# Performance work log

Measured on AMD Instinct MI355X. Metric: run time of the kernel, lower is better.

The kernel has to match this reference:

```python
import jax, jax.numpy as jnp
import numpy as np

EMB = 512      # embedding / LSTM input size
HID = 1024     # LSTM hidden size per direction
NTAGS = 5      # output classes
NWORDS = 50257 # vocab size
T = 4096       # sequence length (batch is hard-coded to 1 in the original)


def setup_inputs() -> dict:
    key = jax.random.key(0)
    ks = jax.random.split(key, 13)
    f32 = jnp.float32

    def gauss(k, shape, scale=0.05):
        return jax.random.normal(k, shape, f32) * scale

    return {
        "words": jax.random.randint(ks[0], (T,), 0, NWORDS),
        # torch.nn.init.uniform_(word_emb.weight, -0.25, 0.25)
        "emb": jax.random.uniform(ks[1], (NWORDS, EMB), f32, -0.25, 0.25),
        # forward-direction LSTM params (PyTorch layout, gate order i,f,g,o)
        "Wih_f": gauss(ks[2], (4 * HID, EMB)),
        "Whh_f": gauss(ks[3], (4 * HID, HID)),
        "bih_f": gauss(ks[4], (4 * HID,)),
        "bhh_f": gauss(ks[5], (4 * HID,)),
        # backward-direction LSTM params
        "Wih_b": gauss(ks[6], (4 * HID, EMB)),
        "Whh_b": gauss(ks[7], (4 * HID, HID)),
        "bih_b": gauss(ks[8], (4 * HID,)),
        "bhh_b": gauss(ks[9], (4 * HID,)),
        # projection Linear(2*HID, NTAGS)
        "Wp": gauss(ks[10], (NTAGS, 2 * HID)),
        "bp": gauss(ks[11], (NTAGS,)),
    }


def _lstm_scan(x, Wih, Whh, bias):
    """Single-direction LSTM over x: [T, E] -> hidden states [T, H]."""
    H = Whh.shape[1]
    # precompute input-to-gate contributions for all timesteps: [T, 4H]
    xg = x @ Wih.T + bias

    def step(carry, g_in):
        h, c = carry
        gates = g_in + h @ Whh.T
        i, f, g, o = jnp.split(gates, 4)
        i = jax.nn.sigmoid(i)
        f = jax.nn.sigmoid(f)
        g = jnp.tanh(g)
        o = jax.nn.sigmoid(o)
        c = f * c + i * g
        h = o * jnp.tanh(c)
        return (h, c), h

    init = (jnp.zeros((H,), x.dtype), jnp.zeros((H,), x.dtype))
    _, hs = jax.lax.scan(step, init, xg)
    return hs


def reference(words, emb, Wih_f, Whh_f, bih_f, bhh_f,
              Wih_b, Whh_b, bih_b, bhh_b, Wp, bp):
    x = emb[words]                                        # [T, E]
    hf = _lstm_scan(x, Wih_f, Whh_f, bih_f + bhh_f)       # [T, H]
    hb = _lstm_scan(x[::-1], Wih_b, Whh_b, bih_b + bhh_b)[::-1]  # [T, H]
    # PyTorch bi-LSTM output[t] = concat(h_fwd[t], h_bwd[t]); take last step
    last = jnp.concatenate([hf[-1], hb[-1]])              # [2H]
    out = last @ Wp.T + bp                                # [NTAGS]
    return out[None, :]                                   # [1, NTAGS]
```

## Files before the change

kernel.cpp:

```cpp
#include <hip/hip_runtime.h>

typedef _Float16 half8 __attribute__((ext_vector_type(8)));
typedef float floatx4 __attribute__((ext_vector_type(4)));
typedef unsigned int u32;
typedef unsigned long long u64;
typedef u64 u64x2 __attribute__((ext_vector_type(2)));

#define T_SEQ 4096
#define EMBD  512
#define HID   1024
#define G4    4096
#define NWG   64


__device__ __forceinline__ void stage16(const void* g, void* l) {
  __builtin_amdgcn_global_load_lds((const __attribute__((address_space(1))) u32*)g,
                                   (__attribute__((address_space(3))) u32*)l, 16, 0, 0);
}

__device__ __forceinline__ float frcp(float x) {
#if __has_builtin(__builtin_amdgcn_rcpf)
  return __builtin_amdgcn_rcpf(x);
#else
  return 1.f / x;
#endif
}

__device__ __forceinline__ float fsigmoid(float x) {
  return frcp(1.f + __expf(-x));
}
__device__ __forceinline__ float ftanh(float x) {
  return fmaf(2.f, frcp(1.f + __expf(-2.f * x)), -1.f);
}


__global__ __launch_bounds__(256) void prep_kernel(
    const float* __restrict__ Whh, const float* __restrict__ Wih,
    const float* __restrict__ emb, const int* __restrict__ words,
    const float* __restrict__ bih, const float* __restrict__ bhh,
    _Float16* __restrict__ whh_h, _Float16* __restrict__ wih_h,
    _Float16* __restrict__ xh, float* __restrict__ biasf, u64* __restrict__ hg) {
  const long long S1 = (long long)G4 * HID;
  const long long S2 = (long long)G4 * EMBD;
  const long long S3 = (long long)T_SEQ * EMBD;
  const long long S4 = G4;
  const long long S5 = 1024;
  const long long tot = S1 + S2 + S3 + S4 + S5;
  long long stride = (long long)gridDim.x * blockDim.x;
  for (long long i = (long long)blockIdx.x * blockDim.x + threadIdx.x; i < tot; i += stride) {
    long long j = i;
    if (j < S1) { whh_h[j] = (_Float16)Whh[j]; continue; }
    j -= S1;
    if (j < S2) { wih_h[j] = (_Float16)Wih[j]; continue; }
    j -= S2;
    if (j < S3) {
      int t = (int)(j >> 9), e = (int)(j & 511);
      xh[j] = (_Float16)emb[(long long)words[t] * EMBD + e];
      continue;
    }
    j -= S3;
    if (j < S4) { biasf[j] = bih[j] + bhh[j]; continue; }
    j -= S4;
    hg[j] = 0ull;
  }
}


__global__ __launch_bounds__(256) void xg_gemm(
    const _Float16* __restrict__ A, const _Float16* __restrict__ B,
    const float* __restrict__ biasf, float* __restrict__ C) {
  __shared__ char smem[2][2][8192];
  const int tid = threadIdx.x;
  const int lane = tid & 63;
  const int wid = tid >> 6;
  const int wy = wid >> 1, wx = wid & 1;
  const int tm = blockIdx.x * 128, tn = blockIdx.y * 128;

  floatx4 acc[4][4];
#pragma unroll
  for (int a = 0; a < 4; a++)
#pragma unroll
    for (int b = 0; b < 4; b++) acc[a][b] = (floatx4){0.f, 0.f, 0.f, 0.f};

  auto stage = [&](int buf, int kb) {
#pragma unroll
    for (int ii = 0; ii < 2; ii++) {
      int ci = tid + ii * 256;
      int r = ci >> 2, cs = ci & 3;
      int c = cs ^ (r & 3);
      const _Float16* srcA = A + (long long)(tm + r) * EMBD + kb + c * 8;
      const _Float16* srcB = B + (long long)(tn + r) * EMBD + kb + c * 8;
      char* ldsA = &smem[buf][0][(ci & ~63) << 4];
      char* ldsB = &smem[buf][1][(ci & ~63) << 4];
      stage16(srcA, ldsA);
      stage16(srcB, ldsB);
    }
  };

  stage(0, 0);
  __syncthreads();

  for (int t = 0; t < 16; t++) {
    int cur = t & 1;
    if (t < 15) stage(cur ^ 1, (t + 1) * 32);
    const char* As = smem[cur][0];
    const char* Bs = smem[cur][1];
    const int kc = lane >> 4;
    half8 af[4], bfr[4];
#pragma unroll
    for (int am = 0; am < 4; am++) {
      int r = wy * 64 + am * 16 + (lane & 15);
      af[am] = *(const half8*)(As + r * 64 + ((kc ^ (r & 3)) << 4));
    }
#pragma unroll
    for (int bn = 0; bn < 4; bn++) {
      int r = wx * 64 + bn * 16 + (lane & 15);
      bfr[bn] = *(const half8*)(Bs + r * 64 + ((kc ^ (r & 3)) << 4));
    }
#pragma unroll
    for (int am = 0; am < 4; am++)
#pragma unroll
      for (int bn = 0; bn < 4; bn++)
        acc[am][bn] = __builtin_amdgcn_mfma_f32_16x16x32_f16(af[am], bfr[bn], acc[am][bn], 0, 0, 0);
    __syncthreads();
  }

#pragma unroll
  for (int am = 0; am < 4; am++) {
    int mrow = tm + wy * 64 + am * 16 + (lane >> 4) * 4;
#pragma unroll
    for (int bn = 0; bn < 4; bn++) {
      int n = tn + wx * 64 + bn * 16 + (lane & 15);
      int r = n & 1023, g = n >> 10;
      int np = ((r >> 4) << 6) + (((r >> 2) & 3) << 4) + ((r & 3) << 2) + g;
      float bias = biasf[n];
#pragma unroll
      for (int rg = 0; rg < 4; rg++)
        C[(long long)(mrow + rg) * G4 + np] = acc[am][bn][rg] + bias;
    }
  }
}


__global__ __launch_bounds__(256, 1) void lstm_fwd(
    const _Float16* __restrict__ Whh_h, const float* __restrict__ xg,
    u64* __restrict__ hg) {
  __shared__ u32 hp[2][512];
  const int tid = threadIdx.x;
  const int lane = tid & 63;
  const int w = tid >> 6;
  const int wg = blockIdx.x;
  const int n = lane & 15;
  const int kc = lane >> 4;

  const int R = (n & 3) * HID + wg * 16 + w * 4 + (n >> 2);
  half8 Wb[32];
  {
    const _Float16* wr = Whh_h + (long long)R * HID + kc * 8;
#pragma unroll
    for (int kk = 0; kk < 32; kk++)
      Wb[kk] = *(const half8*)(wr + kk * 32);
  }

  u64* h0 = hg;
  u64* h1 = hg + 512;
  float c = 0.f;
  const float mulm = ((lane & 3) == 2) ? 2.f : 1.f;
  const float addm = ((lane & 3) == 2) ? -1.f : 0.f;

  const float* xbase = xg + wg * 64 + w * 16 + lane;
  float xv_cur = (lane < 16) ? xbase[0] : 0.f;
  float xv_nxt = 0.f;

  for (int s = 0; s < T_SEQ; s++) {
    const u64* p = ((s & 1) ? h1 : h0) + 2 * tid;
    u64* dst = (s & 1) ? h0 : h1;
    const u32 want = (u32)s;

    u64x2 va, vb, got;
    asm volatile("global_load_dwordx4 %0, %1, off sc1" : "=v"(va) : "v"(p) : "memory");
    asm volatile("global_load_dwordx4 %0, %1, off sc1" : "=v"(vb) : "v"(p) : "memory");
    asm volatile("s_waitcnt vmcnt(2)" ::: "memory");
    __builtin_amdgcn_sched_barrier(0);
    if (__all(((u32)(va.x >> 32) == want) & ((u32)(va.y >> 32) == want))) {
      got = va;
    } else {
      asm volatile("global_load_dwordx4 %0, %1, off sc1" : "=v"(va) : "v"(p) : "memory");
      for (;;) {
        asm volatile("s_waitcnt vmcnt(1)" ::: "memory");
        __builtin_amdgcn_sched_barrier(0);
        if (__all(((u32)(vb.x >> 32) == want) & ((u32)(vb.y >> 32) == want))) { got = vb; break; }
        asm volatile("global_load_dwordx4 %0, %1, off sc1" : "=v"(vb) : "v"(p) : "memory");
        asm volatile("s_waitcnt vmcnt(1)" ::: "memory");
        __builtin_amdgcn_sched_barrier(0);
        if (__all(((u32)(va.x >> 32) == want) & ((u32)(va.y >> 32) == want))) { got = va; break; }
        asm volatile("global_load_dwordx4 %0, %1, off sc1" : "=v"(va) : "v"(p) : "memory");
      }
    }

    u32* hb = hp[s & 1];
    *reinterpret_cast<u64*>(&hb[2 * tid]) = ((u64)(u32)got.y << 32) | (u64)(u32)got.x;
    asm volatile("s_waitcnt lgkmcnt(0)" ::: "memory");
    __builtin_amdgcn_sched_barrier(0);
    __builtin_amdgcn_s_barrier();

    floatx4 ac0 = (floatx4){0.f,0.f,0.f,0.f};
    floatx4 ac1 = (floatx4){0.f,0.f,0.f,0.f};
    floatx4 ac2 = (floatx4){0.f,0.f,0.f,0.f};
    floatx4 ac3 = (floatx4){0.f,0.f,0.f,0.f};
    const char* hh = (const char*)hb;
#pragma unroll
    for (int kb = 0; kb < 8; kb++) {
      half8 a0 = *(const half8*)(hh + (kb * 4 + 0) * 64 + kc * 16);
      half8 a1 = *(const half8*)(hh + (kb * 4 + 1) * 64 + kc * 16);
      half8 a2 = *(const half8*)(hh + (kb * 4 + 2) * 64 + kc * 16);
      half8 a3 = *(const half8*)(hh + (kb * 4 + 3) * 64 + kc * 16);
      ac0 = __builtin_amdgcn_mfma_f32_16x16x32_f16(a0, Wb[kb * 4 + 0], ac0, 0, 0, 0);
      ac1 = __builtin_amdgcn_mfma_f32_16x16x32_f16(a1, Wb[kb * 4 + 1], ac1, 0, 0, 0);
      ac2 = __builtin_amdgcn_mfma_f32_16x16x32_f16(a2, Wb[kb * 4 + 2], ac2, 0, 0, 0);
      ac3 = __builtin_amdgcn_mfma_f32_16x16x32_f16(a3, Wb[kb * 4 + 3], ac3, 0, 0, 0);
    }

    asm volatile("s_waitcnt vmcnt(0)" ::: "memory");
    __builtin_amdgcn_sched_barrier(0);
    asm volatile("" :: "v"(va), "v"(vb));

    if (lane < 16) xv_nxt = xbase[(long long)((s + 1) & (T_SEQ - 1)) * G4];

    float gv = ac0[0] + ac1[0] + ac2[0] + ac3[0] + xv_cur;

    float e = __expf(-(mulm * gv));
    float t = frcp(1.f + e);
    float a = fmaf(t, mulm, addm);
    int base4 = lane & ~3;
    float i_ = __shfl(a, base4 + 0);
    float f_ = __shfl(a, base4 + 1);
    float g_ = __shfl(a, base4 + 2);
    float o_ = __shfl(a, base4 + 3);
    c = fmaf(f_, c, i_ * g_);
    float e2 = __expf(-2.f * c);
    float th = fmaf(2.f, frcp(1.f + e2), -1.f);
    float hn = o_ * th;

    union { _Float16 hx[2]; u32 u; } pk;
    pk.hx[0] = (_Float16)hn; pk.hx[1] = (_Float16)0.f;
    u32 bits = pk.u & 0xffffu;
    u32 nbr = (u32)__shfl((int)bits, lane | 4);
    if (lane < 16 && (lane & 7) == 0) {
      u64 pkt = ((u64)(u32)(s + 1) << 32) | (u64)(bits | ((nbr & 0xffffu) << 16));
      __hip_atomic_store(&dst[wg * 8 + w * 2 + (lane >> 3)], pkt,
                         __ATOMIC_RELAXED, __HIP_MEMORY_SCOPE_AGENT);
    }
    xv_cur = xv_nxt;
  }
}


__global__ __launch_bounds__(256) void bwd_gates(
    const float* __restrict__ Wihb, const float* __restrict__ emb,
    const int* __restrict__ words, const float* __restrict__ bihb,
    const float* __restrict__ bhhb, float* __restrict__ gb) {
  const int row = blockIdx.x * 4 + (threadIdx.x >> 6);
  const int lane = threadIdx.x & 63;
  const long long wl = words[T_SEQ - 1];
  const float* xr = emb + wl * EMBD;
  const float* wr = Wihb + (long long)row * EMBD;
  const int k0 = lane * 8;
  float s = 0.f;
#pragma unroll
  for (int j = 0; j < 8; j += 4) {
    float4 wv = *(const float4*)(wr + k0 + j);
    float4 xv = *(const float4*)(xr + k0 + j);
    s += wv.x * xv.x + wv.y * xv.y + wv.z * xv.z + wv.w * xv.w;
  }
#pragma unroll
  for (int m = 1; m < 64; m <<= 1) s += __shfl_xor(s, m);
  if (lane == 0) gb[row] = s + bihb[row] + bhhb[row];
}


__global__ __launch_bounds__(256) void final_k(
    const u64* __restrict__ hg, const float* __restrict__ gb,
    const float* __restrict__ Wp, const float* __restrict__ bp,
    float* __restrict__ out) {
  __shared__ float last[2 * HID];
  __shared__ float red[4];
  const int tid = threadIdx.x;
  for (int p = tid; p < 512; p += 256) {
    u32 b = (u32)hg[p];
    union { unsigned short s; _Float16 h; } lo, hi;
    lo.s = (unsigned short)(b & 0xffffu);
    hi.s = (unsigned short)(b >> 16);
    last[2 * p]     = (float)lo.h;
    last[2 * p + 1] = (float)hi.h;
  }
  for (int j = tid; j < HID; j += 256) {
    float i_ = fsigmoid(gb[j]);
    float g_ = ftanh(gb[2 * HID + j]);
    float o_ = fsigmoid(gb[3 * HID + j]);
    float cb = i_ * g_;
    last[HID + j] = o_ * ftanh(cb);
  }
  __syncthreads();
  const int lane = tid & 63, wv = tid >> 6;
  for (int nn = 0; nn < 5; nn++) {
    float p = 0.f;
    for (int j = tid; j < 2 * HID; j += 256) p += last[j] * Wp[nn * 2 * HID + j];
#pragma unroll
    for (int m = 1; m < 64; m <<= 1) p += __shfl_xor(p, m);
    if (lane == 0) red[wv] = p;
    __syncthreads();
    if (tid == 0) out[nn] = red[0] + red[1] + red[2] + red[3] + bp[nn];
    __syncthreads();
  }
}


extern "C" void kernel_launch(void* const* d_in, const int* in_sizes, int n_in,
                              void* d_out, int out_size, void* d_ws, size_t ws_size,
                              hipStream_t stream) {
  const int*   words = (const int*)d_in[0];
  const float* emb   = (const float*)d_in[1];
  const float* Wih_f = (const float*)d_in[2];
  const float* Whh_f = (const float*)d_in[3];
  const float* bih_f = (const float*)d_in[4];
  const float* bhh_f = (const float*)d_in[5];
  const float* Wih_b = (const float*)d_in[6];
  const float* bih_b = (const float*)d_in[8];
  const float* bhh_b = (const float*)d_in[9];
  const float* Wp    = (const float*)d_in[10];
  const float* bp    = (const float*)d_in[11];
  float* out = (float*)d_out;

  char* ws = (char*)d_ws;
  float*    XG    = (float*)(ws);
  _Float16* WHH   = (_Float16*)(ws + 67108864);
  _Float16* WIH   = (_Float16*)(ws + 75497472);
  _Float16* XH    = (_Float16*)(ws + 79691776);
  u64*      HG    = (u64*)(ws + 83886080);
  float*    GB    = (float*)(ws + 83902464);
  float*    BIASF = (float*)(ws + 83918848);

  prep_kernel<<<2048, 256, 0, stream>>>(Whh_f, Wih_f, emb, words, bih_f, bhh_f,
                                        WHH, WIH, XH, BIASF, HG);
  xg_gemm<<<dim3(32, 32), 256, 0, stream>>>(XH, WIH, BIASF, XG);
  lstm_fwd<<<NWG, 256, 0, stream>>>(WHH, XG, HG);
  bwd_gates<<<1024, 256, 0, stream>>>(Wih_b, emb, words, bih_b, bhh_b, GB);
  final_k<<<1, 256, 0, stream>>>(HG, GB, Wp, bp, out);
}
```

Baseline: 6.227 ms.

## Elect one XCC for recurrent LSTM workgroups to sync via local L2

```diff
diff --git a/kernel.cpp b/kernel.cpp
--- a/kernel.cpp
+++ b/kernel.cpp
@@ -10,7 +10,6 @@
 #define EMBD  512
 #define HID   1024
 #define G4    4096
-#define NWG   64
 
 
 __device__ __forceinline__ void stage16(const void* g, void* l) {
@@ -39,12 +38,12 @@
     const float* __restrict__ emb, const int* __restrict__ words,
     const float* __restrict__ bih, const float* __restrict__ bhh,
     _Float16* __restrict__ whh_h, _Float16* __restrict__ wih_h,
-    _Float16* __restrict__ xh, float* __restrict__ biasf, u64* __restrict__ hg) {
+    _Float16* __restrict__ xh, float* __restrict__ biasf, u32* __restrict__ elect) {
   const long long S1 = (long long)G4 * HID;
   const long long S2 = (long long)G4 * EMBD;
   const long long S3 = (long long)T_SEQ * EMBD;
   const long long S4 = G4;
-  const long long S5 = 1024;
+  const long long S5 = 64;
   const long long tot = S1 + S2 + S3 + S4 + S5;
   long long stride = (long long)gridDim.x * blockDim.x;
   for (long long i = (long long)blockIdx.x * blockDim.x + threadIdx.x; i < tot; i += stride) {
@@ -61,7 +60,7 @@
     j -= S3;
     if (j < S4) { biasf[j] = bih[j] + bhh[j]; continue; }
     j -= S4;
-    hg[j] = 0ull;
+    elect[j] = (j == 8) ? 0xFFFFFFFFu : 0u;
   }
 }
 
@@ -132,7 +131,7 @@
     for (int bn = 0; bn < 4; bn++) {
       int n = tn + wx * 64 + bn * 16 + (lane & 15);
       int r = n & 1023, g = n >> 10;
-      int np = ((r >> 4) << 6) + (((r >> 2) & 3) << 4) + ((r & 3) << 2) + g;
+      int np = ((r >> 5) << 7) + (((r >> 2) & 7) << 4) + ((r & 3) << 2) + g;
       float bias = biasf[n];
 #pragma unroll
       for (int rg = 0; rg < 4; rg++)
@@ -142,18 +141,42 @@
 }
 
 
-__global__ __launch_bounds__(256, 1) void lstm_fwd(
+__global__ __launch_bounds__(512, 1) void lstm_fwd(
     const _Float16* __restrict__ Whh_h, const float* __restrict__ xg,
-    u64* __restrict__ hg) {
+    u64* __restrict__ hg, u32* __restrict__ elect, float* __restrict__ hf) {
   __shared__ u32 hp[2][512];
+  __shared__ int s_role;
   const int tid = threadIdx.x;
   const int lane = tid & 63;
   const int w = tid >> 6;
-  const int wg = blockIdx.x;
+
+  if (tid == 0) {
+    u32 xcc;
+    asm volatile("s_getreg_b32 %0, hwreg(HW_REG_XCC_ID)" : "=s"(xcc));
+    xcc &= 7u;
+    u32 rank = __hip_atomic_fetch_add(&elect[xcc], 1u, __ATOMIC_RELAXED,
+                                      __HIP_MEMORY_SCOPE_AGENT);
+    if (rank == 31u) {
+      u32 exp = 0xFFFFFFFFu;
+      __hip_atomic_compare_exchange_strong(&elect[8], &exp, xcc,
+          __ATOMIC_RELAXED, __ATOMIC_RELAXED, __HIP_MEMORY_SCOPE_AGENT);
+    }
+    u32 win = 0xFFFFFFFFu;
+    for (int t = 0; t < (1 << 16); t++) {
+      win = __hip_atomic_load(&elect[8], __ATOMIC_RELAXED, __HIP_MEMORY_SCOPE_AGENT);
+      if (win != 0xFFFFFFFFu) break;
+      __builtin_amdgcn_s_sleep(2);
+    }
+    s_role = (win != 0xFFFFFFFFu && win == xcc && rank < 32u) ? (int)rank : -1;
+  }
+  __syncthreads();
+  const int wg = s_role;
+  if (wg < 0) return;
+
   const int n = lane & 15;
   const int kc = lane >> 4;
 
-  const int R = (n & 3) * HID + wg * 16 + w * 4 + (n >> 2);
+  const int R = (n & 3) * HID + wg * 32 + w * 4 + (n >> 2);
   half8 Wb[32];
   {
     const _Float16* wr = Whh_h + (long long)R * HID + kc * 8;
@@ -162,53 +185,89 @@
       Wb[kk] = *(const half8*)(wr + kk * 32);
   }
 
-  u64* h0 = hg;
-  u64* h1 = hg + 512;
+  u64* F0 = hg;
+  u64* F1 = hg + 512;
+  u64* S0 = hg + 1024;
+  u64* S1 = hg + 1536;
+
+  if (tid < 16) {
+    u64 z = 0ull;
+    asm volatile("global_store_dwordx2 %0, %1, off sc0" :: "v"(F0 + wg * 16 + tid), "v"(z) : "memory");
+    asm volatile("global_store_dwordx2 %0, %1, off sc0" :: "v"(F1 + wg * 16 + tid), "v"(z) : "memory");
+    __hip_atomic_store(S0 + wg * 16 + tid, z, __ATOMIC_RELAXED, __HIP_MEMORY_SCOPE_AGENT);
+    __hip_atomic_store(S1 + wg * 16 + tid, z, __ATOMIC_RELAXED, __HIP_MEMORY_SCOPE_AGENT);
+  }
+  __syncthreads();
+
   float c = 0.f;
+  bool slow = false;
   const float mulm = ((lane & 3) == 2) ? 2.f : 1.f;
   const float addm = ((lane & 3) == 2) ? -1.f : 0.f;
 
-  const float* xbase = xg + wg * 64 + w * 16 + lane;
+  const float* xbase = xg + wg * 128 + w * 16 + lane;
   float xv_cur = (lane < 16) ? xbase[0] : 0.f;
   float xv_nxt = 0.f;
 
   for (int s = 0; s < T_SEQ; s++) {
-    const u64* p = ((s & 1) ? h1 : h0) + 2 * tid;
-    u64* dst = (s & 1) ? h0 : h1;
+    const int p = s & 1;
+    u64* Fs = p ? F1 : F0;  u64* Fd = p ? F0 : F1;
+    u64* Ss = p ? S1 : S0;  u64* Sd = p ? S0 : S1;
     const u32 want = (u32)s;
 
-    u64x2 va, vb, got;
-    asm volatile("global_load_dwordx4 %0, %1, off sc1" : "=v"(va) : "v"(p) : "memory");
-    asm volatile("global_load_dwordx4 %0, %1, off sc1" : "=v"(vb) : "v"(p) : "memory");
-    asm volatile("s_waitcnt vmcnt(2)" ::: "memory");
-    __builtin_amdgcn_sched_barrier(0);
-    if (__all(((u32)(va.x >> 32) == want) & ((u32)(va.y >> 32) == want))) {
-      got = va;
-    } else {
-      asm volatile("global_load_dwordx4 %0, %1, off sc1" : "=v"(va) : "v"(p) : "memory");
-      for (;;) {
-        asm volatile("s_waitcnt vmcnt(1)" ::: "memory");
-        __builtin_amdgcn_sched_barrier(0);
-        if (__all(((u32)(vb.x >> 32) == want) & ((u32)(vb.y >> 32) == want))) { got = vb; break; }
-        asm volatile("global_load_dwordx4 %0, %1, off sc1" : "=v"(vb) : "v"(p) : "memory");
-        asm volatile("s_waitcnt vmcnt(1)" ::: "memory");
-        __builtin_amdgcn_sched_barrier(0);
-        if (__all(((u32)(va.x >> 32) == want) & ((u32)(va.y >> 32) == want))) { got = va; break; }
-        asm volatile("global_load_dwordx4 %0, %1, off sc1" : "=v"(va) : "v"(p) : "memory");
+    if (w == 0) {
+      const u64* pf = Fs + 8 * lane;
+      const u64* ps = Ss + 8 * lane;
+      u64x2 q0, q1, q2, q3;
+      bool done = false;
+      if (!slow) {
+        int spins = 0;
+        for (;;) {
+          asm volatile("global_load_dwordx4 %0, %1, off sc0"           : "=v"(q0) : "v"(pf) : "memory");
+          asm volatile("global_load_dwordx4 %0, %1, off offset:16 sc0" : "=v"(q1) : "v"(pf) : "memory");
+          asm volatile("global_load_dwordx4 %0, %1, off offset:32 sc0" : "=v"(q2) : "v"(pf) : "memory");
+          asm volatile("global_load_dwordx4 %0, %1, off offset:48 sc0" : "=v"(q3) : "v"(pf) : "memory");
+          asm volatile("s_waitcnt vmcnt(0)" ::: "memory");
+          __builtin_amdgcn_sched_barrier(0);
+          bool ok = ((u32)(q0.x >> 32) == want) & ((u32)(q0.y >> 32) == want)
+                  & ((u32)(q1.x >> 32) == want) & ((u32)(q1.y >> 32) == want)
+                  & ((u32)(q2.x >> 32) == want) & ((u32)(q2.y >> 32) == want)
+                  & ((u32)(q3.x >> 32) == want) & ((u32)(q3.y >> 32) == want);
+          if (__all(ok)) { done = true; break; }
+          if (++spins > 4096) { slow = true; break; }
+        }
       }
-    }
-
-    u32* hb = hp[s & 1];
-    *reinterpret_cast<u64*>(&hb[2 * tid]) = ((u64)(u32)got.y << 32) | (u64)(u32)got.x;
-    asm volatile("s_waitcnt lgkmcnt(0)" ::: "memory");
-    __builtin_amdgcn_sched_barrier(0);
+      if (!done) {
+        for (;;) {
+          asm volatile("global_load_dwordx4 %0, %1, off sc1"           : "=v"(q0) : "v"(ps) : "memory");
+          asm volatile("global_load_dwordx4 %0, %1, off offset:16 sc1" : "=v"(q1) : "v"(ps) : "memory");
+          asm volatile("global_load_dwordx4 %0, %1, off offset:32 sc1" : "=v"(q2) : "v"(ps) : "memory");
+          asm volatile("global_load_dwordx4 %0, %1, off offset:48 sc1" : "=v"(q3) : "v"(ps) : "memory");
+          asm volatile("s_waitcnt vmcnt(0)" ::: "memory");
+          __builtin_amdgcn_sched_barrier(0);
+          bool ok = ((u32)(q0.x >> 32) == want) & ((u32)(q0.y >> 32) == want)
+                  & ((u32)(q1.x >> 32) == want) & ((u32)(q1.y >> 32) == want)
+                  & ((u32)(q2.x >> 32) == want) & ((u32)(q2.y >> 32) == want)
+                  & ((u32)(q3.x >> 32) == want) & ((u32)(q3.y >> 32) == want);
+          if (__all(ok)) break;
+        }
+      }
+      u32* hb = hp[p];
+      hb[8 * lane + 0] = (u32)q0.x; hb[8 * lane + 1] = (u32)q0.y;
+      hb[8 * lane + 2] = (u32)q1.x; hb[8 * lane + 3] = (u32)q1.y;
+      hb[8 * lane + 4] = (u32)q2.x; hb[8 * lane + 5] = (u32)q2.y;
+      hb[8 * lane + 6] = (u32)q3.x; hb[8 * lane + 7] = (u32)q3.y;
+      asm volatile("s_waitcnt lgkmcnt(0)" ::: "memory");
+      __builtin_amdgcn_sched_barrier(0);
+    }
     __builtin_amdgcn_s_barrier();
+
+    if (lane < 16) xv_nxt = xbase[(long long)((s + 1) & (T_SEQ - 1)) * G4];
 
     floatx4 ac0 = (floatx4){0.f,0.f,0.f,0.f};
     floatx4 ac1 = (floatx4){0.f,0.f,0.f,0.f};
     floatx4 ac2 = (floatx4){0.f,0.f,0.f,0.f};
     floatx4 ac3 = (floatx4){0.f,0.f,0.f,0.f};
-    const char* hh = (const char*)hb;
+    const char* hh = (const char*)hp[p];
 #pragma unroll
     for (int kb = 0; kb < 8; kb++) {
       half8 a0 = *(const half8*)(hh + (kb * 4 + 0) * 64 + kc * 16);
@@ -220,13 +279,6 @@
       ac2 = __builtin_amdgcn_mfma_f32_16x16x32_f16(a2, Wb[kb * 4 + 2], ac2, 0, 0, 0);
       ac3 = __builtin_amdgcn_mfma_f32_16x16x32_f16(a3, Wb[kb * 4 + 3], ac3, 0, 0, 0);
     }
-
-    asm volatile("s_waitcnt vmcnt(0)" ::: "memory");
-    __builtin_amdgcn_sched_barrier(0);
-    asm volatile("" :: "v"(va), "v"(vb));
-
-    if (lane < 16) xv_nxt = xbase[(long long)((s + 1) & (T_SEQ - 1)) * G4];
-
     float gv = ac0[0] + ac1[0] + ac2[0] + ac3[0] + xv_cur;
 
     float e = __expf(-(mulm * gv));
@@ -248,7 +300,12 @@
     u32 nbr = (u32)__shfl((int)bits, lane | 4);
     if (lane < 16 && (lane & 7) == 0) {
       u64 pkt = ((u64)(u32)(s + 1) << 32) | (u64)(bits | ((nbr & 0xffffu) << 16));
-      __hip_atomic_store(&dst[wg * 8 + w * 2 + (lane >> 3)], pkt,
+      const int idx = wg * 16 + w * 2 + (lane >> 3);
+      asm volatile("global_store_dwordx2 %0, %1, off sc0" :: "v"(Fd + idx), "v"(pkt) : "memory");
+      __hip_atomic_store(Sd + idx, pkt, __ATOMIC_RELAXED, __HIP_MEMORY_SCOPE_AGENT);
+    }
+    if (s == T_SEQ - 1 && lane < 16 && (lane & 3) == 0) {
+      __hip_atomic_store(&hf[wg * 32 + w * 4 + (lane >> 2)], hn,
                          __ATOMIC_RELAXED, __HIP_MEMORY_SCOPE_AGENT);
     }
     xv_cur = xv_nxt;
@@ -280,21 +337,14 @@
 
 
 __global__ __launch_bounds__(256) void final_k(
-    const u64* __restrict__ hg, const float* __restrict__ gb,
+    const float* __restrict__ hf, const float* __restrict__ gb,
     const float* __restrict__ Wp, const float* __restrict__ bp,
     float* __restrict__ out) {
   __shared__ float last[2 * HID];
   __shared__ float red[4];
   const int tid = threadIdx.x;
-  for (int p = tid; p < 512; p += 256) {
-    u32 b = (u32)hg[p];
-    union { unsigned short s; _Float16 h; } lo, hi;
-    lo.s = (unsigned short)(b & 0xffffu);
-    hi.s = (unsigned short)(b >> 16);
-    last[2 * p]     = (float)lo.h;
-    last[2 * p + 1] = (float)hi.h;
-  }
   for (int j = tid; j < HID; j += 256) {
+    last[j] = hf[j];
     float i_ = fsigmoid(gb[j]);
     float g_ = ftanh(gb[2 * HID + j]);
     float o_ = fsigmoid(gb[3 * HID + j]);
@@ -338,13 +388,15 @@
   _Float16* WIH   = (_Float16*)(ws + 75497472);
   _Float16* XH    = (_Float16*)(ws + 79691776);
   u64*      HG    = (u64*)(ws + 83886080);
-  float*    GB    = (float*)(ws + 83902464);
-  float*    BIASF = (float*)(ws + 83918848);
+  u32*      ELECT = (u32*)(ws + 83902464);
+  float*    HF    = (float*)(ws + 83918848);
+  float*    GB    = (float*)(ws + 83935232);
+  float*    BIASF = (float*)(ws + 83951616);
 
   prep_kernel<<<2048, 256, 0, stream>>>(Whh_f, Wih_f, emb, words, bih_f, bhh_f,
-                                        WHH, WIH, XH, BIASF, HG);
+                                        WHH, WIH, XH, BIASF, ELECT);
   xg_gemm<<<dim3(32, 32), 256, 0, stream>>>(XH, WIH, BIASF, XG);
-  lstm_fwd<<<NWG, 256, 0, stream>>>(WHH, XG, HG);
+  lstm_fwd<<<256, 512, 0, stream>>>(WHH, XG, HG, ELECT, HF);
   bwd_gates<<<1024, 256, 0, stream>>>(Wih_b, emb, words, bih_b, bhh_b, GB);
-  final_k<<<1, 256, 0, stream>>>(HG, GB, Wp, bp, out);
-}
+  final_k<<<1, 256, 0, stream>>>(HF, GB, Wp, bp, out);
+}
```

Result: slower. 11.62 ms (+86.5%).
